# Kernel tuning notes

Measured on AMD Instinct MI355X. Metric: run time of the kernel, lower is better.

## Reference

```python
import jax, jax.numpy as jnp
import numpy as np

S = 8192   # seq_len (== max_seq_len)
K = 4096   # in_features
N = 4096   # out_features


def setup_inputs() -> dict:
    key = jax.random.key(0)
    k1, k2, k3, k4, k5 = jax.random.split(key, 5)
    # symmetric int8 activations and weights in [-127, 127]
    x = jax.random.randint(k1, (S, K), -127, 128, dtype=jnp.int32).astype(jnp.int8)
    weight_q = jax.random.randint(k2, (N, K), -127, 128, dtype=jnp.int32).astype(jnp.int8)
    # positive dequant scales (per-row symmetric quant: scale = absmax/127)
    scale_x = jax.random.uniform(k3, (S,), minval=0.5, maxval=2.0, dtype=jnp.float32) / 127.0
    scale_w = jax.random.uniform(k4, (N,), minval=0.5, maxval=2.0, dtype=jnp.float32) / 127.0
    # per-output-row requantization scale from the MinMax observer
    scale_y = jax.random.uniform(k5, (S,), minval=0.5, maxval=2.0, dtype=jnp.float32)
    return {"x": x, "weight_q": weight_q, "scale_x": scale_x,
            "scale_w": scale_w, "scale_y": scale_y}


def reference(x, weight_q, scale_x, scale_w, scale_y):
    # int8 GEMM with int32 accumulation: acc[s, n] = sum_k x[s, k] * w[n, k]
    acc = jnp.matmul(x.astype(jnp.int32), weight_q.T.astype(jnp.int32))  # [S, N] int32
    # fused three-scale dequant + requant: (acc * sx[s] * sw[n]) / sy[s]
    scale = (scale_x / scale_y)[:, None] * scale_w[None, :]               # [S, N]
    out_f = acc.astype(jnp.float32) * scale
    out_q = jnp.clip(jnp.round(out_f), -128.0, 127.0).astype(jnp.int8)    # int8 output
    return out_q, scale_y
```

## Files before the change

### kernel.cpp

```cpp
#include <hip/hip_runtime.h>
#include <stdint.h>

#define S_DIM 8192
#define K_DIM 4096
#define N_DIM 4096

#define BM 128
#define BN 256
#define BK 128

typedef int v4i __attribute__((ext_vector_type(4)));

__global__ void prep(const int* __restrict__ x, const int* __restrict__ w,
                     const float* __restrict__ sy,
                     int* __restrict__ dst, float* __restrict__ out) {
    const int nx = S_DIM * K_DIM / 4;
    const int nw = N_DIM * K_DIM / 4;
    int i = blockIdx.x * 256 + threadIdx.x;
    if (i < nx) {
        int4 a = ((const int4*)x)[i];
        dst[i] = (a.x & 0xFF) | ((a.y & 0xFF) << 8) | ((a.z & 0xFF) << 16)
               | ((a.w & 0xFF) << 24);
    } else if (i < nx + nw) {
        int4 a = ((const int4*)w)[i - nx];
        dst[i] = (a.x & 0xFF) | ((a.y & 0xFF) << 8) | ((a.z & 0xFF) << 16)
               | ((a.w & 0xFF) << 24);
    } else {
        int j = i - nx - nw;
        if (j < S_DIM) out[(size_t)S_DIM * N_DIM + j] = sy[j];
    }
}

__global__ void copy_sy(const float* __restrict__ sy, float* __restrict__ out) {
    int i = blockIdx.x * blockDim.x + threadIdx.x;
    if (i < S_DIM) out[(size_t)S_DIM * N_DIM + i] = sy[i];
}

__device__ __forceinline__ void g2lds16(const void* g, void* l) {
    __builtin_amdgcn_global_load_lds((const __attribute__((address_space(1))) void*)g,
                                     (__attribute__((address_space(3))) void*)l,
                                     16, 0, 0);
}

__launch_bounds__(256, 2)
__global__ void gemm_i8(const signed char* __restrict__ xp,
                        const signed char* __restrict__ wp,
                        const float* __restrict__ sx,
                        const float* __restrict__ sw,
                        const float* __restrict__ sy,
                        float* __restrict__ out) {
    __shared__ __align__(16) signed char As[BM * BK];
    __shared__ __align__(16) signed char Bs[BN * BK];

    const int tid  = threadIdx.x;
    const int lane = tid & 63;
    const int quad = lane >> 4;
    const int l16  = lane & 15;
    const int wave = tid >> 6;
    const int wm = wave >> 1;
    const int wn = wave & 1;
    const int bn = blockIdx.x;
    const int bm = blockIdx.y;

    const signed char* aG = xp + (size_t)(bm * BM) * K_DIM;
    const signed char* bG = wp + (size_t)(bn * BN) * K_DIM;

    const int csw = l16 & 7;

    int aOff[4], bOff[8];
#pragma unroll
    for (int i = 0; i < 4; i++) {
        int li = i * 256 + tid;
        int row = li >> 3, c = li & 7, g = c ^ (row & 7);
        aOff[i] = row * K_DIM + (g << 4);
    }
#pragma unroll
    for (int i = 0; i < 8; i++) {
        int li = i * 256 + tid;
        int row = li >> 3, c = li & 7, g = c ^ (row & 7);
        bOff[i] = row * K_DIM + (g << 4);
    }

    v4i acc[4][8];
#pragma unroll
    for (int i = 0; i < 4; i++)
#pragma unroll
        for (int j = 0; j < 8; j++) acc[i][j] = 0;

    for (int kk = 0; kk < K_DIM; kk += BK) {
        __syncthreads();
#pragma unroll
        for (int i = 0; i < 4; i++)
            g2lds16(aG + aOff[i] + kk, As + (i * 256 + tid) * 16);
#pragma unroll
        for (int i = 0; i < 8; i++)
            g2lds16(bG + bOff[i] + kk, Bs + (i * 256 + tid) * 16);
        __syncthreads();

#pragma unroll
        for (int ks = 0; ks < 2; ks++) {
            const int slot = ((ks << 2) | quad) ^ csw;
            v4i af[4], bf[8];
#pragma unroll
            for (int t = 0; t < 4; t++)
                af[t] = *(const v4i*)(As + (wm * 64 + t * 16 + l16) * BK
                                         + (slot << 4));
#pragma unroll
            for (int u = 0; u < 8; u++)
                bf[u] = *(const v4i*)(Bs + (wn * 128 + u * 16 + l16) * BK
                                         + (slot << 4));
#pragma unroll
            for (int mt = 0; mt < 4; mt++)
#pragma unroll
                for (int nt = 0; nt < 8; nt++)
                    acc[mt][nt] = __builtin_amdgcn_mfma_i32_16x16x64_i8(
                        af[mt], bf[nt], acc[mt][nt], 0, 0, 0);
        }
    }

    const int s_base = bm * BM + wm * 64;
    const int n_base = bn * BN + wn * 128;
#pragma unroll
    for (int mt = 0; mt < 4; mt++) {
#pragma unroll
        for (int r = 0; r < 4; r++) {
            int s = s_base + mt * 16 + quad * 4 + r;
            float rs = sx[s] / sy[s];
            float* orow = out + (size_t)s * N_DIM;
#pragma unroll
            for (int nt = 0; nt < 8; nt++) {
                int n = n_base + nt * 16 + l16;
                float v = rintf((float)acc[mt][nt][r] * (rs * sw[n]));
                v = fminf(fmaxf(v, -128.f), 127.f);
                orow[n] = v;
            }
        }
    }
}

__global__ void gemm_naive(const int* __restrict__ x, const int* __restrict__ w,
                           const float* __restrict__ sx, const float* __restrict__ sw,
                           const float* __restrict__ sy, float* __restrict__ out) {
    int n = blockIdx.x * blockDim.x + threadIdx.x;
    int s = blockIdx.y;
    const int4* xr = (const int4*)(x + (size_t)s * K_DIM);
    const int4* wr = (const int4*)(w + (size_t)n * K_DIM);
    int acc = 0;
    for (int k = 0; k < K_DIM / 4; k++) {
        int4 a = xr[k], b = wr[k];
        acc += a.x * b.x + a.y * b.y + a.z * b.z + a.w * b.w;
    }
    float v = rintf((float)acc * (sx[s] / sy[s] * sw[n]));
    out[(size_t)s * N_DIM + n] = fminf(fmaxf(v, -128.f), 127.f);
}

extern "C" void kernel_launch(void* const* d_in, const int* in_sizes, int n_in,
                              void* d_out, int out_size, void* d_ws, size_t ws_size,
                              hipStream_t stream) {
    const int*   x  = (const int*)d_in[0];
    const int*   wq = (const int*)d_in[1];
    const float* sx = (const float*)d_in[2];
    const float* sw = (const float*)d_in[3];
    const float* sy = (const float*)d_in[4];
    float* out = (float*)d_out;

    const size_t need = (size_t)S_DIM * K_DIM + (size_t)N_DIM * K_DIM;
    if (ws_size >= need) {
        signed char* xp = (signed char*)d_ws;
        signed char* wp = xp + (size_t)S_DIM * K_DIM;
        const int nprep = (S_DIM * K_DIM / 4) + (N_DIM * K_DIM / 4) + S_DIM;
        prep<<<dim3((nprep + 255) / 256), dim3(256), 0, stream>>>(
            x, wq, sy, (int*)xp, out);
        gemm_i8<<<dim3(N_DIM / BN, S_DIM / BM), dim3(256), 0, stream>>>(
            xp, wp, sx, sw, sy, out);
    } else {
        copy_sy<<<dim3((S_DIM + 255) / 256), dim3(256), 0, stream>>>(sy, out);
        gemm_naive<<<dim3(N_DIM / 256, S_DIM), dim3(256), 0, stream>>>(
            x, wq, sx, sw, sy, out);
    }
}
```

Baseline: 391.5 us.

## Double-buffer LDS tiles with prefetch and enlarge M tile to 256

```diff
diff --git a/kernel.cpp b/kernel.cpp
--- a/kernel.cpp
+++ b/kernel.cpp
@@ -5,7 +5,7 @@
 #define K_DIM 4096
 #define N_DIM 4096
 
-#define BM 128
+#define BM 256
 #define BN 256
 #define BK 128
 
@@ -42,15 +42,15 @@
                                      16, 0, 0);
 }
 
-__launch_bounds__(256, 2)
+__launch_bounds__(256, 1)
 __global__ void gemm_i8(const signed char* __restrict__ xp,
                         const signed char* __restrict__ wp,
                         const float* __restrict__ sx,
                         const float* __restrict__ sw,
                         const float* __restrict__ sy,
                         float* __restrict__ out) {
-    __shared__ __align__(16) signed char As[BM * BK];
-    __shared__ __align__(16) signed char Bs[BN * BK];
+    __shared__ __align__(16) signed char As[2][BM * BK];
+    __shared__ __align__(16) signed char Bs[2][BN * BK];
 
     const int tid  = threadIdx.x;
     const int lane = tid & 63;
@@ -65,52 +65,57 @@
     const signed char* aG = xp + (size_t)(bm * BM) * K_DIM;
     const signed char* bG = wp + (size_t)(bn * BN) * K_DIM;
 
-    const int csw = l16 & 7;
-
-    int aOff[4], bOff[8];
-#pragma unroll
-    for (int i = 0; i < 4; i++) {
-        int li = i * 256 + tid;
-        int row = li >> 3, c = li & 7, g = c ^ (row & 7);
-        aOff[i] = row * K_DIM + (g << 4);
-    }
+    int sOff[8];
 #pragma unroll
     for (int i = 0; i < 8; i++) {
         int li = i * 256 + tid;
         int row = li >> 3, c = li & 7, g = c ^ (row & 7);
-        bOff[i] = row * K_DIM + (g << 4);
+        sOff[i] = row * K_DIM + (g << 4);
     }
 
-    v4i acc[4][8];
+    v4i acc[8][8];
 #pragma unroll
-    for (int i = 0; i < 4; i++)
+    for (int i = 0; i < 8; i++)
 #pragma unroll
         for (int j = 0; j < 8; j++) acc[i][j] = 0;
 
-    for (int kk = 0; kk < K_DIM; kk += BK) {
+#pragma unroll
+    for (int i = 0; i < 8; i++)
+        g2lds16(aG + sOff[i], &As[0][(i * 256 + tid) * 16]);
+#pragma unroll
+    for (int i = 0; i < 8; i++)
+        g2lds16(bG + sOff[i], &Bs[0][(i * 256 + tid) * 16]);
+
+    const int NSTAGE = K_DIM / BK;
+    for (int s = 0; s < NSTAGE; s++) {
         __syncthreads();
+        if (s + 1 < NSTAGE) {
+            const int kk = (s + 1) * BK;
+            const int b  = (s + 1) & 1;
 #pragma unroll
-        for (int i = 0; i < 4; i++)
-            g2lds16(aG + aOff[i] + kk, As + (i * 256 + tid) * 16);
+            for (int i = 0; i < 8; i++)
+                g2lds16(aG + sOff[i] + kk, &As[b][(i * 256 + tid) * 16]);
 #pragma unroll
-        for (int i = 0; i < 8; i++)
-            g2lds16(bG + bOff[i] + kk, Bs + (i * 256 + tid) * 16);
-        __syncthreads();
+            for (int i = 0; i < 8; i++)
+                g2lds16(bG + sOff[i] + kk, &Bs[b][(i * 256 + tid) * 16]);
+        }
+        const signed char* Ab = As[s & 1];
+        const signed char* Bb = Bs[s & 1];
 
 #pragma unroll
         for (int ks = 0; ks < 2; ks++) {
-            const int slot = ((ks << 2) | quad) ^ csw;
-            v4i af[4], bf[8];
+            const int slot = ((ks << 2) | quad) ^ (l16 & 7);
+            v4i af[8], bf[8];
 #pragma unroll
-            for (int t = 0; t < 4; t++)
-                af[t] = *(const v4i*)(As + (wm * 64 + t * 16 + l16) * BK
+            for (int t = 0; t < 8; t++)
+                af[t] = *(const v4i*)(Ab + (wm * 128 + t * 16 + l16) * BK
                                          + (slot << 4));
 #pragma unroll
             for (int u = 0; u < 8; u++)
-                bf[u] = *(const v4i*)(Bs + (wn * 128 + u * 16 + l16) * BK
+                bf[u] = *(const v4i*)(Bb + (wn * 128 + u * 16 + l16) * BK
                                          + (slot << 4));
 #pragma unroll
-            for (int mt = 0; mt < 4; mt++)
+            for (int mt = 0; mt < 8; mt++)
 #pragma unroll
                 for (int nt = 0; nt < 8; nt++)
                     acc[mt][nt] = __builtin_amdgcn_mfma_i32_16x16x64_i8(
@@ -118,15 +123,15 @@
         }
     }
 
-    const int s_base = bm * BM + wm * 64;
+    const int s_base = bm * BM + wm * 128;
     const int n_base = bn * BN + wn * 128;
 #pragma unroll
-    for (int mt = 0; mt < 4; mt++) {
+    for (int mt = 0; mt < 8; mt++) {
 #pragma unroll
         for (int r = 0; r < 4; r++) {
-            int s = s_base + mt * 16 + quad * 4 + r;
-            float rs = sx[s] / sy[s];
-            float* orow = out + (size_t)s * N_DIM;
+            int srow = s_base + mt * 16 + quad * 4 + r;
+            float rs = sx[srow] / sy[srow];
+            float* orow = out + (size_t)srow * N_DIM;
 #pragma unroll
             for (int nt = 0; nt < 8; nt++) {
                 int n = n_base + nt * 16 + l16;
```

Result: slower. 474.3 us (+21.1%).
